# Optimization experiments

Measured on AMD Instinct MI355X. Metric: run time of the kernel, lower is better.

Reference implementation:

```python
import jax, jax.numpy as jnp
import numpy as np

N_SAMPLES = 128
AGENTS = 64
D = 128          # latent_size
EDIM = 2         # edge attr dim
N = N_SAMPLES * AGENTS
EPS = 1e-5


def _build_edges():
    a = np.arange(AGENTS)
    rows = np.repeat(a, AGENTS)
    cols = np.tile(a, AGENTS)
    mask = rows != cols  # fully connected, no self loops
    rows, cols = rows[mask], cols[mask]
    offsets = (np.arange(N_SAMPLES) * AGENTS)[:, None]
    src = (rows[None, :] + offsets).ravel().astype(np.int32)  # edge_index[0]
    dst = (cols[None, :] + offsets).ravel().astype(np.int32)  # edge_index[1]
    return src, dst


def setup_inputs() -> dict:
    key = jax.random.key(0)
    ks = jax.random.split(key, 16)
    src, dst = _build_edges()
    zin = 2 * D + EDIM  # CGConv concat [x_i, x_j, e]
    inp = {
        "gnn_in": jax.random.normal(ks[0], (N, D), jnp.float32),
        "centers": jax.random.normal(ks[1], (N, EDIM), jnp.float32),
        "edge_src": jnp.asarray(src),
        "edge_dst": jnp.asarray(dst),
    }
    for li, base in ((1, 2), (2, 8)):
        inp[f"Wf{li}"] = jax.random.normal(ks[base + 0], (zin, D), jnp.float32) / np.sqrt(zin)
        inp[f"bf{li}"] = jnp.zeros((D,), jnp.float32)
        inp[f"Ws{li}"] = jax.random.normal(ks[base + 1], (zin, D), jnp.float32) / np.sqrt(zin)
        inp[f"bs{li}"] = jnp.zeros((D,), jnp.float32)
        inp[f"gamma{li}"] = jnp.ones((D,), jnp.float32)
        inp[f"beta{li}"] = jnp.zeros((D,), jnp.float32)
    return inp


def _cgconv(x, e, src, dst, Wf, bf, Ws, bs, gamma, beta):
    # message: z = [x_i(target), x_j(source), e]; sigmoid(Wf z) * softplus(Ws z)
    z = jnp.concatenate([x[dst], x[src], e], axis=-1)  # [E, 2D+2]
    m = jax.nn.sigmoid(z @ Wf + bf) * jax.nn.softplus(z @ Ws + bs)
    agg = jax.ops.segment_sum(m, dst, num_segments=N)  # scatter-add at targets
    # batch norm (training-mode batch stats) then residual, as in PyG CGConv
    mu = agg.mean(axis=0)
    var = agg.var(axis=0)
    agg = (agg - mu) * jax.lax.rsqrt(var + EPS) * gamma + beta
    return agg + x


def reference(gnn_in, centers, edge_src, edge_dst,
              Wf1, bf1, Ws1, bs1, gamma1, beta1,
              Wf2, bf2, Ws2, bs2, gamma2, beta2):
    # edge_attr = centers[col] - centers[row]
    e = centers[edge_dst] - centers[edge_src]  # [E, 2]
    x = jax.nn.relu(_cgconv(gnn_in, e, edge_src, edge_dst, Wf1, bf1, Ws1, bs1, gamma1, beta1))
    x = jax.nn.relu(_cgconv(x, e, edge_src, edge_dst, Wf2, bf2, Ws2, bs2, gamma2, beta2))
    return x
```

## Files before the change

kernel.cpp:

```cpp
#include <hip/hip_runtime.h>
#include <hip/hip_bf16.h>

#define NSAMP 128
#define AGENTS 64
#define D 128
#define NN (NSAMP * AGENTS)
#define LOG2E 1.44269504088896340736f
#define LN2   0.69314718055994530942f
#define EPSF  1e-5f

typedef __attribute__((ext_vector_type(8))) short short8;
typedef __attribute__((ext_vector_type(4))) float floatx4;

__device__ __forceinline__ float u2f(unsigned v) {
    float f; __builtin_memcpy(&f, &v, 4); return f;
}
__device__ __forceinline__ unsigned short f2bf(float f) {
    unsigned x; __builtin_memcpy(&x, &f, 4);
    return (unsigned short)((x + 0x7FFFu + ((x >> 16) & 1u)) >> 16);
}

__global__ __launch_bounds__(256) void cvt_kernel(
    const float* __restrict__ x0,
    const float* __restrict__ Wf1, const float* __restrict__ Ws1,
    const float* __restrict__ Wf2, const float* __restrict__ Ws2,
    unsigned short* __restrict__ Xb, unsigned short* __restrict__ WT,
    float* __restrict__ sacc)
{
    int b = blockIdx.x;
    if (b < 512) {
        int off = (b * 256 + threadIdx.x) * 8;
        float4 v0 = *(const float4*)&x0[off];
        float4 v1 = *(const float4*)&x0[off + 4];
        short8 s;
        s[0] = (short)f2bf(v0.x); s[1] = (short)f2bf(v0.y);
        s[2] = (short)f2bf(v0.z); s[3] = (short)f2bf(v0.w);
        s[4] = (short)f2bf(v1.x); s[5] = (short)f2bf(v1.y);
        s[6] = (short)f2bf(v1.z); s[7] = (short)f2bf(v1.w);
        *(short8*)&Xb[off] = s;
    } else if (b < 576) {
        int wb = b - 512;
        int rr = wb * 16 + (threadIdx.x >> 4);
        int kk = (threadIdx.x & 15) * 8;
        int layer = rr >> 9, rem = rr & 511, arr = rem >> 7, c = rem & 127;
        const float* M = (arr < 2) ? (layer ? Wf2 : Wf1) : (layer ? Ws2 : Ws1);
        int side = arr & 1;
        short8 s;
        #pragma unroll
        for (int j = 0; j < 8; ++j)
            s[j] = (short)f2bf(M[(size_t)(side * 128 + kk + j) * D + c]);
        *(short8*)&WT[(size_t)(layer * 4 + arr) * 16384 + c * 128 + kk] = s;
    } else {
        sacc[threadIdx.x]       = 0.f;
        sacc[256 + threadIdx.x] = 0.f;
    }
}

__global__ __launch_bounds__(256) void prep_edge(
    const unsigned short* __restrict__ Xb,
    const unsigned short* __restrict__ WT,
    const float* __restrict__ centers,
    const float* __restrict__ Wf, const float* __restrict__ bf_,
    const float* __restrict__ Ws, const float* __restrict__ bs_,
    float* __restrict__ agg,
    float* __restrict__ sacc)
{
    const int s = blockIdx.x >> 2, g = blockIdx.x & 3;
    const int nbase = s * AGENTS;
    const int tid = threadIdx.x, wv = tid >> 6, lane = tid & 63;
    const int quad = lane >> 4, l16 = lane & 15;

    __shared__ float        EAls[2][16][132];
    __shared__ unsigned int EBpk[64][132];

    short8 wBf[2][4], wBs[2][4];
    float cwf0[2], cwf1[2], cws0[2], cws1[2], bfv[2], bsv[2];
    #pragma unroll
    for (int p = 0; p < 2; ++p) {
        const int col = wv * 32 + p * 16 + l16;
        const unsigned short* w1 = WT + (size_t)1 * 16384 + (size_t)col * 128 + quad * 8;
        const unsigned short* w3 = WT + (size_t)3 * 16384 + (size_t)col * 128 + quad * 8;
        #pragma unroll
        for (int kc = 0; kc < 4; ++kc) {
            wBf[p][kc] = *(const short8*)(w1 + kc * 32);
            wBs[p][kc] = *(const short8*)(w3 + kc * 32);
        }
        cwf0[p] = Wf[256 * D + col]; cwf1[p] = Wf[257 * D + col];
        cws0[p] = Ws[256 * D + col]; cws1[p] = Ws[257 * D + col];
        bfv[p] = bf_[col]; bsv[p] = bs_[col];
    }

    for (int m = 0; m < 4; ++m) {
        short8 a[4];
        const unsigned short* xr = Xb + (size_t)(nbase + m * 16 + l16) * 128 + quad * 8;
        #pragma unroll
        for (int kc = 0; kc < 4; ++kc) a[kc] = *(const short8*)(xr + kc * 32);
        float ce0[4], ce1[4];
        #pragma unroll
        for (int r = 0; r < 4; ++r) {
            int n = nbase + m * 16 + quad * 4 + r;
            ce0[r] = centers[2 * n]; ce1[r] = centers[2 * n + 1];
        }
        #pragma unroll
        for (int p = 0; p < 2; ++p) {
            floatx4 aF = {0.f,0.f,0.f,0.f}, aS = {0.f,0.f,0.f,0.f};
            #pragma unroll
            for (int kc = 0; kc < 4; ++kc) {
                aF = __builtin_amdgcn_mfma_f32_16x16x32_bf16(a[kc], wBf[p][kc], aF, 0,0,0);
                aS = __builtin_amdgcn_mfma_f32_16x16x32_bf16(a[kc], wBs[p][kc], aS, 0,0,0);
            }
            const int col = wv * 32 + p * 16 + l16;
            #pragma unroll
            for (int r = 0; r < 4; ++r) {
                float ctf = fmaf(ce0[r], cwf0[p], ce1[r] * cwf1[p]);
                float cts = fmaf(ce0[r], cws0[p], ce1[r] * cws1[p]);
                unsigned uf = (unsigned)f2bf(__builtin_amdgcn_exp2f(-LOG2E * (aF[r] - ctf)));
                unsigned us = (unsigned)f2bf(__builtin_amdgcn_exp2f( LOG2E * (aS[r] - cts)));
                EBpk[m * 16 + quad * 4 + r][col] = uf | (us << 16);
            }
        }
        if (m == g) {
            #pragma unroll
            for (int p = 0; p < 2; ++p) {
                const int col = wv * 32 + p * 16 + l16;
                const unsigned short* w0 = WT + (size_t)col * 128 + quad * 8;
                const unsigned short* w2 = WT + (size_t)2 * 16384 + (size_t)col * 128 + quad * 8;
                floatx4 aF = {0.f,0.f,0.f,0.f}, aS = {0.f,0.f,0.f,0.f};
                #pragma unroll
                for (int kc = 0; kc < 4; ++kc) {
                    short8 f0 = *(const short8*)(w0 + kc * 32);
                    short8 f2 = *(const short8*)(w2 + kc * 32);
                    aF = __builtin_amdgcn_mfma_f32_16x16x32_bf16(a[kc], f0, aF, 0,0,0);
                    aS = __builtin_amdgcn_mfma_f32_16x16x32_bf16(a[kc], f2, aS, 0,0,0);
                }
                #pragma unroll
                for (int r = 0; r < 4; ++r) {
                    float ctf = fmaf(ce0[r], cwf0[p], ce1[r] * cwf1[p]);
                    float cts = fmaf(ce0[r], cws0[p], ce1[r] * cws1[p]);
                    EAls[0][quad * 4 + r][col] =
                        __builtin_amdgcn_exp2f(-LOG2E * (aF[r] + ctf + bfv[p]));
                    EAls[1][quad * 4 + r][col] =
                        __builtin_amdgcn_exp2f( LOG2E * (aS[r] + cts + bsv[p]));
                }
            }
        }
    }
    __syncthreads();

    const int c = tid & 127, dh = tid >> 7;
    float eaf[8], eas[8], acc[8];
    #pragma unroll
    for (int i = 0; i < 8; ++i) {
        eaf[i] = EAls[0][dh * 8 + i][c];
        eas[i] = EAls[1][dh * 8 + i][c];
        acc[i] = 0.f;
    }
    for (int j = 0; j < 64; ++j) {
        unsigned pk = EBpk[j][c];
        float ebf = u2f(pk << 16);
        float ebs = u2f(pk & 0xFFFF0000u);
        #pragma unroll
        for (int i = 0; i < 8; ++i) {
            float sg = __builtin_amdgcn_rcpf(fmaf(eaf[i], ebf, 1.f));
            float lg = __builtin_amdgcn_logf(fmaf(eas[i], ebs, 1.f));
            acc[i] = fmaf(sg, lg, acc[i]);
        }
    }
    float s1 = 0.f, s2 = 0.f;
    #pragma unroll
    for (int i = 0; i < 8; ++i) {
        int dl = g * 16 + dh * 8 + i;
        unsigned pk = EBpk[dl][c];
        float ebf = u2f(pk << 16);
        float ebs = u2f(pk & 0xFFFF0000u);
        float sg = __builtin_amdgcn_rcpf(fmaf(eaf[i], ebf, 1.f));
        float lg = __builtin_amdgcn_logf(fmaf(eas[i], ebs, 1.f));
        float a = (acc[i] - sg * lg) * LN2;
        agg[(size_t)(nbase + dl) * D + c] = a;
        s1 += a; s2 += a * a;
    }
    __syncthreads();
    if (dh == 1) { EAls[0][0][c] = s1; EAls[0][1][c] = s2; }
    __syncthreads();
    if (dh == 0) {
        atomicAdd(&sacc[c],       s1 + EAls[0][0][c]);
        atomicAdd(&sacc[128 + c], s2 + EAls[0][1][c]);
    }
}

__global__ __launch_bounds__(256) void bncvt_kernel(
    const float* __restrict__ agg, const float* __restrict__ xin,
    const float* __restrict__ sacc,
    const float* __restrict__ gamma, const float* __restrict__ beta,
    float* __restrict__ x1, unsigned short* __restrict__ Xb)
{
    const int t = blockIdx.x * 256 + threadIdx.x;
    const int n = t >> 4;
    const int c = (t & 15) * 8;
    size_t off = (size_t)n * D + c;
    const float inv = 1.f / NN;
    float v[8]; short8 sv;
    #pragma unroll
    for (int h = 0; h < 2; ++h) {
        float4 a  = *(const float4*)&agg[off + h * 4];
        float4 xv = *(const float4*)&xin[off + h * 4];
        float4 s1 = *(const float4*)&sacc[c + h * 4];
        float4 s2 = *(const float4*)&sacc[128 + c + h * 4];
        float4 gm = *(const float4*)&gamma[c + h * 4];
        float4 bt = *(const float4*)&beta[c + h * 4];
        float mu, var, rs;
        mu = s1.x * inv; var = s2.x * inv - mu * mu; rs = rsqrtf(var + EPSF);
        v[h*4+0] = fmaxf(0.f, fmaf((a.x - mu) * rs, gm.x, bt.x) + xv.x);
        mu = s1.y * inv; var = s2.y * inv - mu * mu; rs = rsqrtf(var + EPSF);
        v[h*4+1] = fmaxf(0.f, fmaf((a.y - mu) * rs, gm.y, bt.y) + xv.y);
        mu = s1.z * inv; var = s2.z * inv - mu * mu; rs = rsqrtf(var + EPSF);
        v[h*4+2] = fmaxf(0.f, fmaf((a.z - mu) * rs, gm.z, bt.z) + xv.z);
        mu = s1.w * inv; var = s2.w * inv - mu * mu; rs = rsqrtf(var + EPSF);
        v[h*4+3] = fmaxf(0.f, fmaf((a.w - mu) * rs, gm.w, bt.w) + xv.w);
    }
    *(float4*)&x1[off]     = *(float4*)&v[0];
    *(float4*)&x1[off + 4] = *(float4*)&v[4];
    #pragma unroll
    for (int e = 0; e < 8; ++e) sv[e] = (short)f2bf(v[e]);
    *(short8*)&Xb[off] = sv;
}

__global__ __launch_bounds__(256) void bn_kernel(
    const float* __restrict__ agg, const float* __restrict__ xin,
    const float* __restrict__ sacc,
    const float* __restrict__ gamma, const float* __restrict__ beta,
    float* __restrict__ outp)
{
    const int t = blockIdx.x * 256 + threadIdx.x;
    const int n = t >> 4;
    const int c = (t & 15) * 8;
    size_t off = (size_t)n * D + c;
    const float inv = 1.f / NN;
    float v[8];
    #pragma unroll
    for (int h = 0; h < 2; ++h) {
        float4 a  = *(const float4*)&agg[off + h * 4];
        float4 xv = *(const float4*)&xin[off + h * 4];
        float4 s1 = *(const float4*)&sacc[c + h * 4];
        float4 s2 = *(const float4*)&sacc[128 + c + h * 4];
        float4 gm = *(const float4*)&gamma[c + h * 4];
        float4 bt = *(const float4*)&beta[c + h * 4];
        float mu, var, rs;
        mu = s1.x * inv; var = s2.x * inv - mu * mu; rs = rsqrtf(var + EPSF);
        v[h*4+0] = fmaxf(0.f, fmaf((a.x - mu) * rs, gm.x, bt.x) + xv.x);
        mu = s1.y * inv; var = s2.y * inv - mu * mu; rs = rsqrtf(var + EPSF);
        v[h*4+1] = fmaxf(0.f, fmaf((a.y - mu) * rs, gm.y, bt.y) + xv.y);
        mu = s1.z * inv; var = s2.z * inv - mu * mu; rs = rsqrtf(var + EPSF);
        v[h*4+2] = fmaxf(0.f, fmaf((a.z - mu) * rs, gm.z, bt.z) + xv.z);
        mu = s1.w * inv; var = s2.w * inv - mu * mu; rs = rsqrtf(var + EPSF);
        v[h*4+3] = fmaxf(0.f, fmaf((a.w - mu) * rs, gm.w, bt.w) + xv.w);
    }
    *(float4*)&outp[off]     = *(float4*)&v[0];
    *(float4*)&outp[off + 4] = *(float4*)&v[4];
}

extern "C" void kernel_launch(void* const* d_in, const int* in_sizes, int n_in,
                              void* d_out, int out_size, void* d_ws, size_t ws_size,
                              hipStream_t stream) {
    const float* x0      = (const float*)d_in[0];
    const float* centers = (const float*)d_in[1];
    const float* Wf[2] = { (const float*)d_in[4],  (const float*)d_in[10] };
    const float* bf[2] = { (const float*)d_in[5],  (const float*)d_in[11] };
    const float* Ws[2] = { (const float*)d_in[6],  (const float*)d_in[12] };
    const float* bs[2] = { (const float*)d_in[7],  (const float*)d_in[13] };
    const float* gm[2] = { (const float*)d_in[8],  (const float*)d_in[14] };
    const float* bt[2] = { (const float*)d_in[9],  (const float*)d_in[15] };

    const size_t ND = (size_t)NN * D;
    unsigned short* ws_u = (unsigned short*)d_ws;
    unsigned short* Xb = ws_u;
    unsigned short* WT = ws_u + ND;
    float* fbase = (float*)(WT + 2 * 65536);
    float* agg   = fbase;
    float* x1    = fbase + ND;
    float* sacc  = fbase + 2 * ND;

    float* outp = (float*)d_out;

    cvt_kernel<<<dim3(577), dim3(256), 0, stream>>>(
        x0, Wf[0], Ws[0], Wf[1], Ws[1], Xb, WT, sacc);

    prep_edge<<<dim3(512), dim3(256), 0, stream>>>(
        Xb, WT, centers, Wf[0], bf[0], Ws[0], bs[0], agg, sacc);
    bncvt_kernel<<<dim3(512), dim3(256), 0, stream>>>(
        agg, x0, sacc, gm[0], bt[0], x1, Xb);

    prep_edge<<<dim3(512), dim3(256), 0, stream>>>(
        Xb, WT + 65536, centers, Wf[1], bf[1], Ws[1], bs[1], agg, sacc + 256);
    bn_kernel<<<dim3(512), dim3(256), 0, stream>>>(
        agg, x1, sacc + 256, gm[1], bt[1], outp);
}
```

Measured before the change: 163.1 us.

## Split each sample across eight blocks, pack target terms to bf16, cut registers

Result: slower. 219.8 us (+34.8%).

```diff
diff --git a/kernel.cpp b/kernel.cpp
--- a/kernel.cpp
+++ b/kernel.cpp
@@ -14,6 +14,9 @@
 
 __device__ __forceinline__ float u2f(unsigned v) {
     float f; __builtin_memcpy(&f, &v, 4); return f;
+}
+__device__ __forceinline__ unsigned f2u(float f) {
+    unsigned v; __builtin_memcpy(&v, &f, 4); return v;
 }
 __device__ __forceinline__ unsigned short f2bf(float f) {
     unsigned x; __builtin_memcpy(&x, &f, 4);
@@ -56,7 +59,7 @@
     }
 }
 
-__global__ __launch_bounds__(256) void prep_edge(
+__global__ __launch_bounds__(256, 4) void prep_edge(
     const unsigned short* __restrict__ Xb,
     const unsigned short* __restrict__ WT,
     const float* __restrict__ centers,
@@ -65,30 +68,23 @@
     float* __restrict__ agg,
     float* __restrict__ sacc)
 {
-    const int s = blockIdx.x >> 2, g = blockIdx.x & 3;
+    const int s = blockIdx.x >> 3, g = blockIdx.x & 7;
     const int nbase = s * AGENTS;
     const int tid = threadIdx.x, wv = tid >> 6, lane = tid & 63;
     const int quad = lane >> 4, l16 = lane & 15;
 
-    __shared__ float        EAls[2][16][132];
-    __shared__ unsigned int EBpk[64][132];
-
-    short8 wBf[2][4], wBs[2][4];
+    __shared__ unsigned int EBpk[64][128];
+    __shared__ unsigned int EApk[16][128];
+
     float cwf0[2], cwf1[2], cws0[2], cws1[2], bfv[2], bsv[2];
     #pragma unroll
     for (int p = 0; p < 2; ++p) {
         const int col = wv * 32 + p * 16 + l16;
-        const unsigned short* w1 = WT + (size_t)1 * 16384 + (size_t)col * 128 + quad * 8;
-        const unsigned short* w3 = WT + (size_t)3 * 16384 + (size_t)col * 128 + quad * 8;
-        #pragma unroll
-        for (int kc = 0; kc < 4; ++kc) {
-            wBf[p][kc] = *(const short8*)(w1 + kc * 32);
-            wBs[p][kc] = *(const short8*)(w3 + kc * 32);
-        }
         cwf0[p] = Wf[256 * D + col]; cwf1[p] = Wf[257 * D + col];
         cws0[p] = Ws[256 * D + col]; cws1[p] = Ws[257 * D + col];
         bfv[p] = bf_[col]; bsv[p] = bs_[col];
     }
+    const int mg = g >> 1;
 
     for (int m = 0; m < 4; ++m) {
         short8 a[4];
@@ -103,13 +99,15 @@
         }
         #pragma unroll
         for (int p = 0; p < 2; ++p) {
+            const int col = wv * 32 + p * 16 + l16;
+            const unsigned short* w1 = WT + (size_t)1 * 16384 + (size_t)col * 128 + quad * 8;
+            const unsigned short* w3 = WT + (size_t)3 * 16384 + (size_t)col * 128 + quad * 8;
             floatx4 aF = {0.f,0.f,0.f,0.f}, aS = {0.f,0.f,0.f,0.f};
             #pragma unroll
             for (int kc = 0; kc < 4; ++kc) {
-                aF = __builtin_amdgcn_mfma_f32_16x16x32_bf16(a[kc], wBf[p][kc], aF, 0,0,0);
-                aS = __builtin_amdgcn_mfma_f32_16x16x32_bf16(a[kc], wBs[p][kc], aS, 0,0,0);
+                aF = __builtin_amdgcn_mfma_f32_16x16x32_bf16(a[kc], *(const short8*)(w1 + kc * 32), aF, 0,0,0);
+                aS = __builtin_amdgcn_mfma_f32_16x16x32_bf16(a[kc], *(const short8*)(w3 + kc * 32), aS, 0,0,0);
             }
-            const int col = wv * 32 + p * 16 + l16;
             #pragma unroll
             for (int r = 0; r < 4; ++r) {
                 float ctf = fmaf(ce0[r], cwf0[p], ce1[r] * cwf1[p]);
@@ -119,7 +117,7 @@
                 EBpk[m * 16 + quad * 4 + r][col] = uf | (us << 16);
             }
         }
-        if (m == g) {
+        if (m == mg) {
             #pragma unroll
             for (int p = 0; p < 2; ++p) {
                 const int col = wv * 32 + p * 16 + l16;
@@ -128,19 +126,16 @@
                 floatx4 aF = {0.f,0.f,0.f,0.f}, aS = {0.f,0.f,0.f,0.f};
                 #pragma unroll
                 for (int kc = 0; kc < 4; ++kc) {
-                    short8 f0 = *(const short8*)(w0 + kc * 32);
-                    short8 f2 = *(const short8*)(w2 + kc * 32);
-                    aF = __builtin_amdgcn_mfma_f32_16x16x32_bf16(a[kc], f0, aF, 0,0,0);
-                    aS = __builtin_amdgcn_mfma_f32_16x16x32_bf16(a[kc], f2, aS, 0,0,0);
+                    aF = __builtin_amdgcn_mfma_f32_16x16x32_bf16(a[kc], *(const short8*)(w0 + kc * 32), aF, 0,0,0);
+                    aS = __builtin_amdgcn_mfma_f32_16x16x32_bf16(a[kc], *(const short8*)(w2 + kc * 32), aS, 0,0,0);
                 }
                 #pragma unroll
                 for (int r = 0; r < 4; ++r) {
                     float ctf = fmaf(ce0[r], cwf0[p], ce1[r] * cwf1[p]);
                     float cts = fmaf(ce0[r], cws0[p], ce1[r] * cws1[p]);
-                    EAls[0][quad * 4 + r][col] =
-                        __builtin_amdgcn_exp2f(-LOG2E * (aF[r] + ctf + bfv[p]));
-                    EAls[1][quad * 4 + r][col] =
-                        __builtin_amdgcn_exp2f( LOG2E * (aS[r] + cts + bsv[p]));
+                    unsigned uf = (unsigned)f2bf(__builtin_amdgcn_exp2f(-LOG2E * (aF[r] + ctf + bfv[p])));
+                    unsigned us = (unsigned)f2bf(__builtin_amdgcn_exp2f( LOG2E * (aS[r] + cts + bsv[p])));
+                    EApk[quad * 4 + r][col] = uf | (us << 16);
                 }
             }
         }
@@ -148,19 +143,22 @@
     __syncthreads();
 
     const int c = tid & 127, dh = tid >> 7;
-    float eaf[8], eas[8], acc[8];
-    #pragma unroll
-    for (int i = 0; i < 8; ++i) {
-        eaf[i] = EAls[0][dh * 8 + i][c];
-        eas[i] = EAls[1][dh * 8 + i][c];
+    const int r0 = (g & 1) * 8 + dh * 4;
+    float eaf[4], eas[4], acc[4];
+    #pragma unroll
+    for (int i = 0; i < 4; ++i) {
+        unsigned pk = EApk[r0 + i][c];
+        eaf[i] = u2f(pk << 16);
+        eas[i] = u2f(pk & 0xFFFF0000u);
         acc[i] = 0.f;
     }
+    #pragma unroll 2
     for (int j = 0; j < 64; ++j) {
         unsigned pk = EBpk[j][c];
         float ebf = u2f(pk << 16);
         float ebs = u2f(pk & 0xFFFF0000u);
         #pragma unroll
-        for (int i = 0; i < 8; ++i) {
+        for (int i = 0; i < 4; ++i) {
             float sg = __builtin_amdgcn_rcpf(fmaf(eaf[i], ebf, 1.f));
             float lg = __builtin_amdgcn_logf(fmaf(eas[i], ebs, 1.f));
             acc[i] = fmaf(sg, lg, acc[i]);
@@ -168,8 +166,8 @@
     }
     float s1 = 0.f, s2 = 0.f;
     #pragma unroll
-    for (int i = 0; i < 8; ++i) {
-        int dl = g * 16 + dh * 8 + i;
+    for (int i = 0; i < 4; ++i) {
+        int dl = g * 8 + dh * 4 + i;
         unsigned pk = EBpk[dl][c];
         float ebf = u2f(pk << 16);
         float ebs = u2f(pk & 0xFFFF0000u);
@@ -180,11 +178,11 @@
         s1 += a; s2 += a * a;
     }
     __syncthreads();
-    if (dh == 1) { EAls[0][0][c] = s1; EAls[0][1][c] = s2; }
+    if (dh == 1) { EApk[0][c] = f2u(s1); EApk[1][c] = f2u(s2); }
     __syncthreads();
     if (dh == 0) {
-        atomicAdd(&sacc[c],       s1 + EAls[0][0][c]);
-        atomicAdd(&sacc[128 + c], s2 + EAls[0][1][c]);
+        atomicAdd(&sacc[c],       s1 + u2f(EApk[0][c]));
+        atomicAdd(&sacc[128 + c], s2 + u2f(EApk[1][c]));
     }
 }
 
@@ -285,12 +283,12 @@
     cvt_kernel<<<dim3(577), dim3(256), 0, stream>>>(
         x0, Wf[0], Ws[0], Wf[1], Ws[1], Xb, WT, sacc);
 
-    prep_edge<<<dim3(512), dim3(256), 0, stream>>>(
+    prep_edge<<<dim3(1024), dim3(256), 0, stream>>>(
         Xb, WT, centers, Wf[0], bf[0], Ws[0], bs[0], agg, sacc);
     bncvt_kernel<<<dim3(512), dim3(256), 0, stream>>>(
         agg, x0, sacc, gm[0], bt[0], x1, Xb);
 
-    prep_edge<<<dim3(512), dim3(256), 0, stream>>>(
+    prep_edge<<<dim3(1024), dim3(256), 0, stream>>>(
         Xb, WT + 65536, centers, Wf[1], bf[1], Ws[1], bs[1], agg, sacc + 256);
     bn_kernel<<<dim3(512), dim3(256), 0, stream>>>(
         agg, x1, sacc + 256, gm[1], bt[1], outp);
```
